# Kernel tuning notes

Measured on AMD Instinct MI355X. Metric: run time of the kernel, lower is better.

Reference implementation:

```python
import jax, jax.numpy as jnp
import numpy as np

NUM_CLASSES = 5  # the torch module hard-codes 5 center buckets
EPS = 1e-08


def setup_inputs() -> dict:
    key = jax.random.key(0)
    k1, k2 = jax.random.split(key)
    B, C = 262144, 512
    inp = jax.random.normal(k1, (B, C), dtype=jnp.float32)
    # large B with 5 classes -> every class is populated (matches the
    # common-path torch behavior where all center shapes are [C])
    target = jax.random.randint(k2, (B,), 0, NUM_CLASSES, dtype=jnp.int64)
    return {"input": inp, "target": target}


def _centers(inp, target):
    # per-sample softmax (use_act=True), then scatter-mean by class id
    probs = jax.nn.softmax(inp, axis=-1)                              # [B, C]
    sums = jax.ops.segment_sum(probs, target, num_segments=NUM_CLASSES)   # [5, C]
    counts = jax.ops.segment_sum(
        jnp.ones(inp.shape[0], dtype=inp.dtype), target, num_segments=NUM_CLASSES
    )                                                                  # [5]
    counts = jnp.maximum(counts, 1.0)
    return sums / counts[:, None]                                     # [5, C]


def reference(input, target):
    centers = _centers(input, target)
    # MSELoss with default 'mean' reduction
    mse01 = jnp.mean((centers[0] - centers[1]) ** 2)
    mse23 = jnp.mean((centers[2] - centers[3]) ** 2)
    loss = EPS + (1.0 - mse01) + (1.0 - mse23)
    return jnp.reshape(loss, (1,))  # torch returns a [1]-shaped tensor
```

## Files before the change

### kernel.cpp

```cpp
#include <hip/hip_runtime.h>

#define NCLS  4
#define NC    512
#define EPSF  1e-08f
#define NSLOT 8
#define SLOT  2056

__global__ __launch_bounds__(256) void k_accum(const float* __restrict__ inp,
                                               const int*   __restrict__ tgt2,
                                               float* __restrict__ sums8,
                                               int B) {
    __shared__ float lsum[NCLS * NC];
    __shared__ float lcnt[NCLS];
    for (int i = threadIdx.x; i < NCLS * NC; i += blockDim.x) lsum[i] = 0.0f;
    if (threadIdx.x < NCLS) lcnt[threadIdx.x] = 0.0f;
    __syncthreads();

    const int lane = threadIdx.x & 63;
    const int wib  = threadIdx.x >> 6;
    const int gw   = blockIdx.x * 4 + wib;
    const int row0 = gw * 64;

    int tv = NCLS;
    if (row0 + lane < B) tv = tgt2[2 * (size_t)(row0 + lane)];

    unsigned long long mask = __ballot(tv < NCLS);
    float cntv[NCLS];
#pragma unroll
    for (int k = 0; k < NCLS; ++k)
        cntv[k] = (float)__popcll(__ballot(tv == k));

    float acc[NCLS][8];
#pragma unroll
    for (int k = 0; k < NCLS; ++k)
#pragma unroll
        for (int j = 0; j < 8; ++j) acc[k][j] = 0.0f;

#define EXP4(v) v.x = __expf(v.x); v.y = __expf(v.y); v.z = __expf(v.z); v.w = __expf(v.w)

    while (mask) {
        const int i0 = __builtin_ctzll(mask); mask &= mask - 1;
        if (mask) {
            const int i1 = __builtin_ctzll(mask); mask &= mask - 1;
            const float4* p0 = (const float4*)(inp + (size_t)(row0 + i0) * NC);
            const float4* p1 = (const float4*)(inp + (size_t)(row0 + i1) * NC);
            float4 a0 = p0[lane]; float4 b0 = p0[lane + 64];
            float4 a1 = p1[lane]; float4 b1 = p1[lane + 64];
            const int t0 = __builtin_amdgcn_readlane(tv, i0);
            const int t1 = __builtin_amdgcn_readlane(tv, i1);

            EXP4(a0); EXP4(b0); EXP4(a1); EXP4(b1);
            float s0 = ((a0.x + a0.y) + (a0.z + a0.w)) + ((b0.x + b0.y) + (b0.z + b0.w));
            float s1 = ((a1.x + a1.y) + (a1.z + a1.w)) + ((b1.x + b1.y) + (b1.z + b1.w));
#pragma unroll
            for (int off = 32; off > 0; off >>= 1) {
                s0 += __shfl_xor(s0, off, 64);
                s1 += __shfl_xor(s1, off, 64);
            }
            const float inv0 = 1.0f / s0;
            const float inv1 = 1.0f / s1;
#pragma unroll
            for (int k = 0; k < NCLS; ++k) {
                const float w0 = (t0 == k) ? inv0 : 0.0f;
                const float w1 = (t1 == k) ? inv1 : 0.0f;
                acc[k][0] += a0.x * w0 + a1.x * w1;
                acc[k][1] += a0.y * w0 + a1.y * w1;
                acc[k][2] += a0.z * w0 + a1.z * w1;
                acc[k][3] += a0.w * w0 + a1.w * w1;
                acc[k][4] += b0.x * w0 + b1.x * w1;
                acc[k][5] += b0.y * w0 + b1.y * w1;
                acc[k][6] += b0.z * w0 + b1.z * w1;
                acc[k][7] += b0.w * w0 + b1.w * w1;
            }
        } else {
            const float4* p0 = (const float4*)(inp + (size_t)(row0 + i0) * NC);
            float4 a0 = p0[lane]; float4 b0 = p0[lane + 64];
            const int t0 = __builtin_amdgcn_readlane(tv, i0);
            EXP4(a0); EXP4(b0);
            float s0 = ((a0.x + a0.y) + (a0.z + a0.w)) + ((b0.x + b0.y) + (b0.z + b0.w));
#pragma unroll
            for (int off = 32; off > 0; off >>= 1) s0 += __shfl_xor(s0, off, 64);
            const float inv0 = 1.0f / s0;
#pragma unroll
            for (int k = 0; k < NCLS; ++k) {
                const float w = (t0 == k) ? inv0 : 0.0f;
                acc[k][0] += a0.x * w; acc[k][1] += a0.y * w;
                acc[k][2] += a0.z * w; acc[k][3] += a0.w * w;
                acc[k][4] += b0.x * w; acc[k][5] += b0.y * w;
                acc[k][6] += b0.z * w; acc[k][7] += b0.w * w;
            }
        }
    }
#undef EXP4

#pragma unroll
    for (int k = 0; k < NCLS; ++k) {
#pragma unroll
        for (int j = 0; j < 4; ++j) {
            atomicAdd(&lsum[k * NC + 4 * lane + j],       acc[k][j]);
            atomicAdd(&lsum[k * NC + 256 + 4 * lane + j], acc[k][4 + j]);
        }
    }
    if (lane == 0) {
#pragma unroll
        for (int k = 0; k < NCLS; ++k) atomicAdd(&lcnt[k], cntv[k]);
    }
    __syncthreads();

    float* dst = sums8 + (size_t)(blockIdx.x & (NSLOT - 1)) * SLOT;
    for (int i = threadIdx.x; i < NCLS * NC; i += blockDim.x)
        atomicAdd(&dst[i], lsum[i]);
    if (threadIdx.x < NCLS)
        atomicAdd(&dst[NCLS * NC + threadIdx.x], lcnt[threadIdx.x]);
}

__global__ __launch_bounds__(512) void k_final(const float* __restrict__ sums8,
                                               float* __restrict__ out) {
    __shared__ float csh[4];
    __shared__ float red[16];
    const int tid = threadIdx.x;

    if (tid < 4) {
        float c = 0.0f;
#pragma unroll
        for (int s = 0; s < NSLOT; ++s) c += sums8[s * SLOT + NCLS * NC + tid];
        csh[tid] = fmaxf(c, 1.0f);
    }
    __syncthreads();
    const float r0 = 1.0f / csh[0];
    const float r1 = 1.0f / csh[1];
    const float r2 = 1.0f / csh[2];
    const float r3 = 1.0f / csh[3];

    float s0 = 0.f, s1 = 0.f, s2 = 0.f, s3 = 0.f;
#pragma unroll
    for (int s = 0; s < NSLOT; ++s) {
        const float* sg = sums8 + s * SLOT;
        s0 += sg[0 * NC + tid];
        s1 += sg[1 * NC + tid];
        s2 += sg[2 * NC + tid];
        s3 += sg[3 * NC + tid];
    }
    const float d01 = s0 * r0 - s1 * r1;
    const float d23 = s2 * r2 - s3 * r3;
    float q01 = d01 * d01;
    float q23 = d23 * d23;
#pragma unroll
    for (int off = 32; off > 0; off >>= 1) {
        q01 += __shfl_xor(q01, off, 64);
        q23 += __shfl_xor(q23, off, 64);
    }
    const int w = tid >> 6;
    if ((tid & 63) == 0) { red[w] = q01; red[8 + w] = q23; }
    __syncthreads();
    if (tid == 0) {
        float a = 0.f, b = 0.f;
#pragma unroll
        for (int i = 0; i < 8; ++i) { a += red[i]; b += red[8 + i]; }
        const float mse01 = a * (1.0f / (float)NC);
        const float mse23 = b * (1.0f / (float)NC);
        out[0] = EPSF + (1.0f - mse01) + (1.0f - mse23);
    }
}

extern "C" void kernel_launch(void* const* d_in, const int* in_sizes, int n_in,
                              void* d_out, int out_size, void* d_ws, size_t ws_size,
                              hipStream_t stream) {
    const float* inp  = (const float*)d_in[0];
    const int*   tgt2 = (const int*)d_in[1];
    float* out = (float*)d_out;
    const int B = in_sizes[1];

    float* sums8 = (float*)d_ws;
    hipMemsetAsync(d_ws, 0, NSLOT * SLOT * sizeof(float), stream);

    const int waves  = (B + 63) / 64;
    const int blocks = (waves + 3) / 4;
    k_accum<<<blocks, 256, 0, stream>>>(inp, tgt2, sums8, B);
    k_final<<<1, 512, 0, stream>>>(sums8, out);
}
```

Measured before the change: 127.8 us.

## Halve rows per wave, drop two-row unrolling, and raise occupancy hint

Each wave now processes 32 rows instead of 64, which doubles the number of blocks. The two-row unrolled inner loop is replaced by a single-row loop, and launch_bounds now asks for 8 blocks per CU. The intent is lower register pressure and higher occupancy so that more loads are in flight and memory latency is better hidden. The cost is twice as many per-block LDS reductions and global atomic flushes, plus less instruction-level parallelism inside each wave.

```diff
diff --git a/kernel.cpp b/kernel.cpp
--- a/kernel.cpp
+++ b/kernel.cpp
@@ -5,11 +5,12 @@
 #define EPSF  1e-08f
 #define NSLOT 8
 #define SLOT  2056
+#define RPW   32
 
-__global__ __launch_bounds__(256) void k_accum(const float* __restrict__ inp,
-                                               const int*   __restrict__ tgt2,
-                                               float* __restrict__ sums8,
-                                               int B) {
+__global__ __launch_bounds__(256, 8) void k_accum(const float* __restrict__ inp,
+                                                  const int*   __restrict__ tgt2,
+                                                  float* __restrict__ sums8,
+                                                  int B) {
     __shared__ float lsum[NCLS * NC];
     __shared__ float lcnt[NCLS];
     for (int i = threadIdx.x; i < NCLS * NC; i += blockDim.x) lsum[i] = 0.0f;
@@ -19,10 +20,10 @@
     const int lane = threadIdx.x & 63;
     const int wib  = threadIdx.x >> 6;
     const int gw   = blockIdx.x * 4 + wib;
-    const int row0 = gw * 64;
+    const int row0 = gw * RPW;
 
     int tv = NCLS;
-    if (row0 + lane < B) tv = tgt2[2 * (size_t)(row0 + lane)];
+    if (lane < RPW && row0 + lane < B) tv = tgt2[2 * (size_t)(row0 + lane)];
 
     unsigned long long mask = __ballot(tv < NCLS);
     float cntv[NCLS];
@@ -36,62 +37,29 @@
 #pragma unroll
         for (int j = 0; j < 8; ++j) acc[k][j] = 0.0f;
 
-#define EXP4(v) v.x = __expf(v.x); v.y = __expf(v.y); v.z = __expf(v.z); v.w = __expf(v.w)
-
     while (mask) {
         const int i0 = __builtin_ctzll(mask); mask &= mask - 1;
-        if (mask) {
-            const int i1 = __builtin_ctzll(mask); mask &= mask - 1;
-            const float4* p0 = (const float4*)(inp + (size_t)(row0 + i0) * NC);
-            const float4* p1 = (const float4*)(inp + (size_t)(row0 + i1) * NC);
-            float4 a0 = p0[lane]; float4 b0 = p0[lane + 64];
-            float4 a1 = p1[lane]; float4 b1 = p1[lane + 64];
-            const int t0 = __builtin_amdgcn_readlane(tv, i0);
-            const int t1 = __builtin_amdgcn_readlane(tv, i1);
+        const float4* p = (const float4*)(inp + (size_t)(row0 + i0) * NC);
+        float4 a = p[lane];
+        float4 b = p[lane + 64];
+        const int t = __builtin_amdgcn_readlane(tv, i0);
 
-            EXP4(a0); EXP4(b0); EXP4(a1); EXP4(b1);
-            float s0 = ((a0.x + a0.y) + (a0.z + a0.w)) + ((b0.x + b0.y) + (b0.z + b0.w));
-            float s1 = ((a1.x + a1.y) + (a1.z + a1.w)) + ((b1.x + b1.y) + (b1.z + b1.w));
+        a.x = __expf(a.x); a.y = __expf(a.y); a.z = __expf(a.z); a.w = __expf(a.w);
+        b.x = __expf(b.x); b.y = __expf(b.y); b.z = __expf(b.z); b.w = __expf(b.w);
+        float s = ((a.x + a.y) + (a.z + a.w)) + ((b.x + b.y) + (b.z + b.w));
 #pragma unroll
-            for (int off = 32; off > 0; off >>= 1) {
-                s0 += __shfl_xor(s0, off, 64);
-                s1 += __shfl_xor(s1, off, 64);
-            }
-            const float inv0 = 1.0f / s0;
-            const float inv1 = 1.0f / s1;
+        for (int off = 32; off > 0; off >>= 1) s += __shfl_xor(s, off, 64);
+        const float inv = 1.0f / s;
+
 #pragma unroll
-            for (int k = 0; k < NCLS; ++k) {
-                const float w0 = (t0 == k) ? inv0 : 0.0f;
-                const float w1 = (t1 == k) ? inv1 : 0.0f;
-                acc[k][0] += a0.x * w0 + a1.x * w1;
-                acc[k][1] += a0.y * w0 + a1.y * w1;
-                acc[k][2] += a0.z * w0 + a1.z * w1;
-                acc[k][3] += a0.w * w0 + a1.w * w1;
-                acc[k][4] += b0.x * w0 + b1.x * w1;
-                acc[k][5] += b0.y * w0 + b1.y * w1;
-                acc[k][6] += b0.z * w0 + b1.z * w1;
-                acc[k][7] += b0.w * w0 + b1.w * w1;
-            }
-        } else {
-            const float4* p0 = (const float4*)(inp + (size_t)(row0 + i0) * NC);
-            float4 a0 = p0[lane]; float4 b0 = p0[lane + 64];
-            const int t0 = __builtin_amdgcn_readlane(tv, i0);
-            EXP4(a0); EXP4(b0);
-            float s0 = ((a0.x + a0.y) + (a0.z + a0.w)) + ((b0.x + b0.y) + (b0.z + b0.w));
-#pragma unroll
-            for (int off = 32; off > 0; off >>= 1) s0 += __shfl_xor(s0, off, 64);
-            const float inv0 = 1.0f / s0;
-#pragma unroll
-            for (int k = 0; k < NCLS; ++k) {
-                const float w = (t0 == k) ? inv0 : 0.0f;
-                acc[k][0] += a0.x * w; acc[k][1] += a0.y * w;
-                acc[k][2] += a0.z * w; acc[k][3] += a0.w * w;
-                acc[k][4] += b0.x * w; acc[k][5] += b0.y * w;
-                acc[k][6] += b0.z * w; acc[k][7] += b0.w * w;
-            }
+        for (int k = 0; k < NCLS; ++k) {
+            const float w = (t == k) ? inv : 0.0f;
+            acc[k][0] += a.x * w; acc[k][1] += a.y * w;
+            acc[k][2] += a.z * w; acc[k][3] += a.w * w;
+            acc[k][4] += b.x * w; acc[k][5] += b.y * w;
+            acc[k][6] += b.z * w; acc[k][7] += b.w * w;
         }
     }
-#undef EXP4
 
 #pragma unroll
     for (int k = 0; k < NCLS; ++k) {
@@ -174,7 +142,7 @@
     float* sums8 = (float*)d_ws;
     hipMemsetAsync(d_ws, 0, NSLOT * SLOT * sizeof(float), stream);
 
-    const int waves  = (B + 63) / 64;
+    const int waves  = (B + RPW - 1) / RPW;
     const int blocks = (waves + 3) / 4;
     k_accum<<<blocks, 256, 0, stream>>>(inp, tgt2, sums8, B);
     k_final<<<1, 512, 0, stream>>>(sums8, out);
```

Measured after the change: 163.0 us. 1.28x slower.
